# Kernel optimization log

Measured on AMD Instinct MI355X. Metric: run time of the kernel, lower is better.

The kernel has to match this reference:

```python
import jax, jax.numpy as jnp
import numpy as np

EPS = 1e-6  # eigenvalue floor before log

def _gauss_1d(sigma):
    r = int(np.ceil(3.0 * sigma))
    t = np.arange(-r, r + 1, dtype=np.float32)
    g = np.exp(-0.5 * (t / sigma) ** 2)
    g = g / g.sum()
    dg = (-t / (sigma ** 2)) * g  # derivative-of-gaussian kernel
    return jnp.asarray(g), jnp.asarray(dg)

def _conv_axis(x, k, axis):
    # x: [N, 1, D, H, W]; 1D conv along given spatial axis (2,3,4), SAME padding
    K = k.shape[0]
    wshape = [1, 1, 1, 1, 1]; wshape[axis] = K
    w = k.reshape(wshape)
    pad = [(0, 0)] * 3; pad[axis - 2] = (K // 2, K // 2)
    return jax.lax.conv_general_dilated(
        x, w, (1, 1, 1), pad,
        dimension_numbers=('NCDHW', 'OIDHW', 'NCDHW'))

def _blur3(x, g):
    return _conv_axis(_conv_axis(_conv_axis(x, g, 4), g, 3), g, 2)

def _structure_tensor(v, sigma, rho):
    # v: [B, 1, D, H, W] -> per-voxel symmetric 3x3 tensor [B, D, H, W, 3, 3]
    g_s, dg_s = _gauss_1d(sigma)
    g_r, _ = _gauss_1d(rho)
    # derivative-of-gaussian gradients (separable)
    gx = _conv_axis(_conv_axis(_conv_axis(v, dg_s, 4), g_s, 3), g_s, 2)
    gy = _conv_axis(_conv_axis(_conv_axis(v, g_s, 4), dg_s, 3), g_s, 2)
    gz = _conv_axis(_conv_axis(_conv_axis(v, g_s, 4), g_s, 3), dg_s, 2)
    # 6 unique components Sxx,Syy,Szz,Sxy,Sxz,Syz, blurred at scale rho
    comps = jnp.concatenate(
        [gx * gx, gy * gy, gz * gz, gx * gy, gx * gz, gy * gz], axis=1)  # [B,6,D,H,W]
    B, _, D, H, W = comps.shape
    comps = _blur3(comps.reshape(B * 6, 1, D, H, W), g_r).reshape(B, 6, D, H, W)
    Sxx, Syy, Szz, Sxy, Sxz, Syz = [comps[:, i] for i in range(6)]
    row0 = jnp.stack([Sxx, Sxy, Sxz], axis=-1)
    row1 = jnp.stack([Sxy, Syy, Syz], axis=-1)
    row2 = jnp.stack([Sxz, Syz, Szz], axis=-1)
    return jnp.stack([row0, row1, row2], axis=-2)  # [B,D,H,W,3,3]

def _logm_sym(M):
    # matrix log of batched symmetric 3x3 via eigendecomposition
    w, V = jnp.linalg.eigh(M)
    logw = jnp.log(jnp.maximum(w, EPS))
    return jnp.einsum('...ij,...j,...kj->...ik', V, logw, V)

def setup_inputs() -> dict:
    key = jax.random.key(0)
    k1, k2 = jax.random.split(key)
    shape = (2, 1, 96, 96, 96)
    return {
        'real_hi_res': jax.random.normal(k1, shape, dtype=jnp.float32),
        'fake_hi_res': jax.random.normal(k2, shape, dtype=jnp.float32),
    }

def reference(real_hi_res, fake_hi_res, sigma=1.0, rho=2.0):
    S_real = _structure_tensor(real_hi_res, sigma, rho)
    S_fake = _structure_tensor(fake_hi_res, sigma, rho)
    L_real = _logm_sym(S_real)
    L_fake = _logm_sym(S_fake)
    diff = L_real - L_fake
    # per-voxel squared log-Euclidean distance, mean per patch, summed over batch
    dist_points = jnp.sum(diff * diff, axis=(-2, -1))  # [B,D,H,W]
    loss = jnp.sum(jnp.mean(dist_points, axis=(1, 2, 3)))
    return loss
```

## Files before the change

### kernel.cpp

```cpp
#include <hip/hip_runtime.h>
#include <math.h>

#define DIM 96
#define HW_ 9216
#define N3 884736
#define TPB 256

template<int K> struct CW { float w[K]; };

__device__ inline float4 ld4(const float* p) { return *reinterpret_cast<const float4*>(p); }
__device__ inline void st4(float* p, float4 v) { *reinterpret_cast<float4*>(p) = v; }
__device__ inline float2 ld2(const float* p) { return *reinterpret_cast<const float2*>(p); }
__device__ inline float4 fma4(float w, float4 a, float4 acc) {
  acc.x = fmaf(w, a.x, acc.x); acc.y = fmaf(w, a.y, acc.y);
  acc.z = fmaf(w, a.z, acc.z); acc.w = fmaf(w, a.w, acc.w); return acc;
}
__device__ inline float2 fma2(float w, float2 a, float2 acc) {
  acc.x = fmaf(w, a.x, acc.x); acc.y = fmaf(w, a.y, acc.y); return acc;
}
__device__ inline int xswz(int bid, int nb) { return (bid & 7) * (nb >> 3) + (bid >> 3); }

__global__ void k1_dualW(const float* __restrict__ p0, const float* __restrict__ p1,
                         const float* __restrict__ p2, const float* __restrict__ p3,
                         float* __restrict__ A, int nvol, CW<7> g, CW<7> dg) {
  int t = blockIdx.x * TPB + threadIdx.x;
  if (t >= nvol * (N3 / 4)) return;
  int base = t * 4;
  int v = base / N3, i = base - v * N3;
  const float* src = (v == 0) ? p0 : (v == 1) ? p1 : (v == 2) ? p2 : p3;
  int x = i % DIM;
  float win[10];
#pragma unroll
  for (int u = 0; u < 10; ++u) {
    int xx = x + u - 3;
    win[u] = (0 <= xx && xx < DIM) ? src[i + u - 3] : 0.f;
  }
  float4 sa, sb;
#pragma unroll
  for (int k = 0; k < 4; ++k) {
    float a_ = 0.f, b_ = 0.f;
#pragma unroll
    for (int j = 0; j < 7; ++j) {
      float val = win[k + j];
      a_ = fmaf(g.w[j], val, a_);
      b_ = fmaf(dg.w[j], val, b_);
    }
    ((float*)&sa)[k] = a_;
    ((float*)&sb)[k] = b_;
  }
  st4(A + (size_t)(2 * v) * N3 + i, sa);
  st4(A + (size_t)(2 * v + 1) * N3 + i, sb);
}

__global__ void k2_H(const float* __restrict__ A, float* __restrict__ B,
                     int nvol, CW<7> g, CW<7> dg) {
  int t = blockIdx.x * TPB + threadIdx.x;
  if (t >= nvol * (N3 / 4)) return;
  int base = t * 4;
  int v = base / N3, i = base - v * N3;
  int h = (i / DIM) % DIM;
  const float* Wg  = A + (size_t)(2 * v) * N3;
  const float* Wdg = A + (size_t)(2 * v + 1) * N3;
  float4 t0 = {0,0,0,0}, t1 = {0,0,0,0}, t2 = {0,0,0,0};
#pragma unroll
  for (int j = -3; j <= 3; ++j) {
    int hh = h + j;
    if (0 <= hh && hh < DIM) {
      float4 a = ld4(Wg + i + j * DIM);
      t0 = fma4(g.w[j + 3], a, t0);
      t1 = fma4(dg.w[j + 3], a, t1);
      float4 b = ld4(Wdg + i + j * DIM);
      t2 = fma4(g.w[j + 3], b, t2);
    }
  }
  st4(B + (size_t)(3 * v + 0) * N3 + i, t0);
  st4(B + (size_t)(3 * v + 1) * N3 + i, t1);
  st4(B + (size_t)(3 * v + 2) * N3 + i, t2);
}

__global__ void k3_D(const float* __restrict__ B, float* __restrict__ A,
                     int nf, CW<7> g, CW<7> dg) {
  int t = xswz(blockIdx.x, gridDim.x) * TPB + threadIdx.x;
  if (t >= nf * (N3 / 4)) return;
  int base = t * 4;
  int f = base / N3;
  int d = (base / HW_) % DIM;
  bool use_dg = (f % 3 == 0);
  float4 acc = {0,0,0,0};
#pragma unroll
  for (int j = -3; j <= 3; ++j) {
    int dd = d + j;
    if (0 <= dd && dd < DIM) {
      float w = use_dg ? dg.w[j + 3] : g.w[j + 3];
      acc = fma4(w, ld4(B + base + j * HW_), acc);
    }
  }
  st4(A + base, acc);
}

__global__ void k4_prodW(const float* __restrict__ A, float* __restrict__ C,
                         int nvol, CW<13> w13) {
  int t = blockIdx.x * TPB + threadIdx.x;
  if (t >= nvol * (N3 / 4)) return;
  int base = t * 4;
  int v = base / N3, i = base - v * N3;
  const float* gz = A + (size_t)(3 * v + 0) * N3;
  const float* gy = A + (size_t)(3 * v + 1) * N3;
  const float* gx = A + (size_t)(3 * v + 2) * N3;
  int x = i % DIM;
  float wx[16], wy[16], wz[16];
#pragma unroll
  for (int u = 0; u < 16; ++u) {
    int xx = x + u - 6;
    bool ok = (0 <= xx && xx < DIM);
    wx[u] = ok ? gx[i + u - 6] : 0.f;
    wy[u] = ok ? gy[i + u - 6] : 0.f;
    wz[u] = ok ? gz[i + u - 6] : 0.f;
  }
  float4 a0 = {0,0,0,0}, a1 = {0,0,0,0}, a2 = {0,0,0,0};
  float4 a3 = {0,0,0,0}, a4 = {0,0,0,0}, a5 = {0,0,0,0};
#pragma unroll
  for (int k = 0; k < 4; ++k) {
    float s0=0,s1=0,s2=0,s3=0,s4=0,s5=0;
#pragma unroll
    for (int j = 0; j < 13; ++j) {
      float w = w13.w[j];
      float a = wx[k + j], b = wy[k + j], c = wz[k + j];
      float wa = w * a, wb = w * b, wc = w * c;
      s0 = fmaf(wa, a, s0); s3 = fmaf(wa, b, s3); s4 = fmaf(wa, c, s4);
      s1 = fmaf(wb, b, s1); s5 = fmaf(wb, c, s5);
      s2 = fmaf(wc, c, s2);
    }
    ((float*)&a0)[k]=s0; ((float*)&a1)[k]=s1; ((float*)&a2)[k]=s2;
    ((float*)&a3)[k]=s3; ((float*)&a4)[k]=s4; ((float*)&a5)[k]=s5;
  }
  float* dst = C + (size_t)(6 * v) * N3;
  st4(dst + 0*N3 + i, a0); st4(dst + 1*N3 + i, a1); st4(dst + 2*N3 + i, a2);
  st4(dst + 3*N3 + i, a3); st4(dst + 4*N3 + i, a4); st4(dst + 5*N3 + i, a5);
}

__global__ void k5_blurD(const float* __restrict__ In, float* __restrict__ Out,
                         int nf, CW<13> w13) {
  int t = xswz(blockIdx.x, gridDim.x) * TPB + threadIdx.x;
  if (t >= nf * (N3 / 4)) return;
  int base = t * 4;
  int d = (base / HW_) % DIM;
  float4 acc = {0,0,0,0};
#pragma unroll
  for (int j = -6; j <= 6; ++j) {
    int dd = d + j;
    if (0 <= dd && dd < DIM)
      acc = fma4(w13.w[j + 6], ld4(In + base + j * HW_), acc);
  }
  st4(Out + base, acc);
}

template<int P, int Q, int RR>
__device__ inline void jrot(float a[3][3], float V[3][3]) {
  float apq = a[P][Q];
  if (apq != 0.f) {
    float app = a[P][P], aqq = a[Q][Q];
    float theta = 0.5f * (aqq - app) / apq;
    float t = 1.f / (fabsf(theta) + sqrtf(theta * theta + 1.f));
    t = (theta >= 0.f) ? t : -t;
    float c = rsqrtf(t * t + 1.f);
    float s = t * c;
    a[P][P] = app - t * apq;
    a[Q][Q] = aqq + t * apq;
    a[P][Q] = 0.f; a[Q][P] = 0.f;
    float arp = a[RR][P], arq = a[RR][Q];
    float nrp = c * arp - s * arq;
    float nrq = s * arp + c * arq;
    a[RR][P] = nrp; a[P][RR] = nrp;
    a[RR][Q] = nrq; a[Q][RR] = nrq;
#pragma unroll
    for (int r = 0; r < 3; ++r) {
      float vp = V[r][P], vq = V[r][Q];
      V[r][P] = c * vp - s * vq;
      V[r][Q] = s * vp + c * vq;
    }
  }
}

__device__ inline void logm3(const float s6[6], float L[6]) {
  float a[3][3] = {{s6[0], s6[3], s6[4]},
                   {s6[3], s6[1], s6[5]},
                   {s6[4], s6[5], s6[2]}};
  float V[3][3] = {{1,0,0},{0,1,0},{0,0,1}};
#pragma unroll
  for (int sw = 0; sw < 4; ++sw) {
    jrot<0,1,2>(a, V);
    jrot<0,2,1>(a, V);
    jrot<1,2,0>(a, V);
  }
  float l0 = logf(fmaxf(a[0][0], 1e-6f));
  float l1 = logf(fmaxf(a[1][1], 1e-6f));
  float l2 = logf(fmaxf(a[2][2], 1e-6f));
  L[0] = l0*V[0][0]*V[0][0] + l1*V[0][1]*V[0][1] + l2*V[0][2]*V[0][2];
  L[1] = l0*V[1][0]*V[1][0] + l1*V[1][1]*V[1][1] + l2*V[1][2]*V[1][2];
  L[2] = l0*V[2][0]*V[2][0] + l1*V[2][1]*V[2][1] + l2*V[2][2]*V[2][2];
  L[3] = l0*V[0][0]*V[1][0] + l1*V[0][1]*V[1][1] + l2*V[0][2]*V[1][2];
  L[4] = l0*V[0][0]*V[2][0] + l1*V[0][1]*V[2][1] + l2*V[0][2]*V[2][2];
  L[5] = l0*V[1][0]*V[2][0] + l1*V[1][1]*V[2][1] + l2*V[1][2]*V[2][2];
}

__global__ void k6_fused(const float* __restrict__ Sr, const float* __restrict__ Sf,
                         size_t strideElems, int nb, float* __restrict__ out,
                         CW<13> w13) {
  int t = xswz(blockIdx.x, gridDim.x) * TPB + threadIdx.x;
  float val = 0.f;
  if (t < nb * (N3 / 2)) {
    int b = t / (N3 / 2);
    int base = (t - b * (N3 / 2)) * 2;
    int h = (base / DIM) % DIM;
    const float* sR = Sr + (size_t)b * strideElems;
    const float* sF = Sf + (size_t)b * strideElems;
    float2 sr[6], sf[6];
#pragma unroll
    for (int c = 0; c < 6; ++c) {
      float2 ar = {0,0}, af = {0,0};
#pragma unroll
      for (int j = -6; j <= 6; ++j) {
        int hh = h + j;
        if (0 <= hh && hh < DIM) {
          float w = w13.w[j + 6];
          ar = fma2(w, ld2(sR + (size_t)c * N3 + base + j * DIM), ar);
          af = fma2(w, ld2(sF + (size_t)c * N3 + base + j * DIM), af);
        }
      }
      sr[c] = ar; sf[c] = af;
    }
#pragma unroll
    for (int k = 0; k < 2; ++k) {
      float s6r[6], s6f[6], Lr[6], Lf[6];
#pragma unroll
      for (int c = 0; c < 6; ++c) {
        s6r[c] = ((const float*)&sr[c])[k];
        s6f[c] = ((const float*)&sf[c])[k];
      }
      logm3(s6r, Lr);
      logm3(s6f, Lf);
      float d0 = Lr[0]-Lf[0], d1 = Lr[1]-Lf[1], d2 = Lr[2]-Lf[2];
      float d3 = Lr[3]-Lf[3], d4 = Lr[4]-Lf[4], d5 = Lr[5]-Lf[5];
      val += d0*d0 + d1*d1 + d2*d2 + 2.f*(d3*d3 + d4*d4 + d5*d5);
    }
  }
#pragma unroll
  for (int off = 32; off > 0; off >>= 1) val += __shfl_down(val, off, 64);
  __shared__ float sm[TPB / 64];
  int wave = threadIdx.x >> 6;
  if ((threadIdx.x & 63) == 0) sm[wave] = val;
  __syncthreads();
  if (threadIdx.x == 0) {
    float s = 0.f;
#pragma unroll
    for (int wv = 0; wv < TPB / 64; ++wv) s += sm[wv];
    atomicAdd(out, s * (1.0f / (float)N3));
  }
}

extern "C" void kernel_launch(void* const* d_in, const int* in_sizes, int n_in,
                              void* d_out, int out_size, void* d_ws, size_t ws_size,
                              hipStream_t stream) {
  const float* real = (const float*)d_in[0];
  const float* fake = (const float*)d_in[1];
  float* out = (float*)d_out;

  CW<7> g7, d7;
  CW<13> g13;
  {
    double g[7], sum = 0.0;
    for (int i = 0; i < 7; ++i) { double t = i - 3; g[i] = exp(-0.5 * t * t); sum += g[i]; }
    for (int i = 0; i < 7; ++i) {
      double gn = g[i] / sum;
      g7.w[i] = (float)gn;
      d7.w[i] = (float)(-(double)(i - 3) * gn);
    }
    double h[13], s2 = 0.0;
    for (int i = 0; i < 13; ++i) { double t = (i - 6) / 2.0; h[i] = exp(-0.5 * t * t); s2 += h[i]; }
    for (int i = 0; i < 13; ++i) g13.w[i] = (float)(h[i] / s2);
  }

  hipMemsetAsync(d_out, 0, sizeof(float) * (size_t)out_size, stream);

  const size_t FLD = (size_t)N3;
  float* W = (float*)d_ws;

  const size_t need_fused = 48 * FLD * sizeof(float);
  if (ws_size >= need_fused) {
    float* A = W;
    float* B = A + 12 * FLD;
    float* C = B + 12 * FLD;
    const int gV  = 4 * (N3 / 4) / TPB;
    const int g12 = 12 * (N3 / 4) / TPB;
    const int g24 = 24 * (N3 / 4) / TPB;
    const int g6  = 2 * (N3 / 2) / TPB;

    k1_dualW<<<gV,  TPB, 0, stream>>>(real, fake, real + N3, fake + N3, A, 4, g7, d7);
    k2_H    <<<gV,  TPB, 0, stream>>>(A, B, 4, g7, d7);
    k3_D    <<<g12, TPB, 0, stream>>>(B, A, 12, g7, d7);
    k4_prodW<<<gV,  TPB, 0, stream>>>(A, C, 4, g13);
    k5_blurD<<<g24, TPB, 0, stream>>>(C, W, 24, g13);
    k6_fused<<<g6,  TPB, 0, stream>>>(W, W + 6 * FLD, 12 * FLD, 2, out, g13);
  } else {
    float* P0 = W;
    float* P1 = P0 + 6 * FLD;
    float* P2 = P1 + 6 * FLD;
    const int gV  = 2 * (N3 / 4) / TPB;
    const int g6  = 6 * (N3 / 4) / TPB;
    const int gK6 = 1 * (N3 / 2) / TPB;

    for (int b = 0; b < 2; ++b) {
      const float* rv = real + (size_t)b * N3;
      const float* fv = fake + (size_t)b * N3;
      k1_dualW<<<gV, TPB, 0, stream>>>(rv, fv, rv, fv, P0, 2, g7, d7);
      k2_H    <<<gV, TPB, 0, stream>>>(P0, P1, 2, g7, d7);
      k3_D    <<<g6, TPB, 0, stream>>>(P1, P0, 6, g7, d7);
      k4_prodW<<<gV, TPB, 0, stream>>>(P0, P1, 2, g13);
      k5_blurD<<<g6, TPB, 0, stream>>>(P1, P0, 6, g13);
      k5_blurD<<<g6, TPB, 0, stream>>>(P2, P1, 6, g13);
      k6_fused<<<gK6, TPB, 0, stream>>>(P0, P1, 0, 1, out, g13);
    }
  }
}
```

Baseline: 382.1 us.

## Replace Jacobi eigensolver with closed-form eigenvalues and Sylvester polynomial logm

Replaces the 4-sweep Jacobi rotation eigendecomposition in the per-voxel 3x3 matrix log with closed-form trigonometric eigenvalues. The log is then built as a quadratic matrix polynomial in S using divided differences, so no eigenvectors are needed. This removes many divisions, square roots and data-dependent branches from the fused logm kernel. It relies on fast intrinsics (__cosf, __logf, __frcp_rn) and fallback branches for near-degenerate eigenvalues, which adds some risk to numerical accuracy.

Result: faster. 354.1 us (-7.3%).

```diff
diff --git a/kernel.cpp b/kernel.cpp
--- a/kernel.cpp
+++ b/kernel.cpp
@@ -5,6 +5,7 @@
 #define HW_ 9216
 #define N3 884736
 #define TPB 256
+#define EPSF 1e-6f
 
 template<int K> struct CW { float w[K]; };
 
@@ -155,53 +156,61 @@
   st4(Out + base, acc);
 }
 
-template<int P, int Q, int RR>
-__device__ inline void jrot(float a[3][3], float V[3][3]) {
-  float apq = a[P][Q];
-  if (apq != 0.f) {
-    float app = a[P][P], aqq = a[Q][Q];
-    float theta = 0.5f * (aqq - app) / apq;
-    float t = 1.f / (fabsf(theta) + sqrtf(theta * theta + 1.f));
-    t = (theta >= 0.f) ? t : -t;
-    float c = rsqrtf(t * t + 1.f);
-    float s = t * c;
-    a[P][P] = app - t * apq;
-    a[Q][Q] = aqq + t * apq;
-    a[P][Q] = 0.f; a[Q][P] = 0.f;
-    float arp = a[RR][P], arq = a[RR][Q];
-    float nrp = c * arp - s * arq;
-    float nrq = s * arp + c * arq;
-    a[RR][P] = nrp; a[P][RR] = nrp;
-    a[RR][Q] = nrq; a[Q][RR] = nrq;
-#pragma unroll
-    for (int r = 0; r < 3; ++r) {
-      float vp = V[r][P], vq = V[r][Q];
-      V[r][P] = c * vp - s * vq;
-      V[r][Q] = s * vp + c * vq;
-    }
-  }
-}
-
 __device__ inline void logm3(const float s6[6], float L[6]) {
-  float a[3][3] = {{s6[0], s6[3], s6[4]},
-                   {s6[3], s6[1], s6[5]},
-                   {s6[4], s6[5], s6[2]}};
-  float V[3][3] = {{1,0,0},{0,1,0},{0,0,1}};
-#pragma unroll
-  for (int sw = 0; sw < 4; ++sw) {
-    jrot<0,1,2>(a, V);
-    jrot<0,2,1>(a, V);
-    jrot<1,2,0>(a, V);
-  }
-  float l0 = logf(fmaxf(a[0][0], 1e-6f));
-  float l1 = logf(fmaxf(a[1][1], 1e-6f));
-  float l2 = logf(fmaxf(a[2][2], 1e-6f));
-  L[0] = l0*V[0][0]*V[0][0] + l1*V[0][1]*V[0][1] + l2*V[0][2]*V[0][2];
-  L[1] = l0*V[1][0]*V[1][0] + l1*V[1][1]*V[1][1] + l2*V[1][2]*V[1][2];
-  L[2] = l0*V[2][0]*V[2][0] + l1*V[2][1]*V[2][1] + l2*V[2][2]*V[2][2];
-  L[3] = l0*V[0][0]*V[1][0] + l1*V[0][1]*V[1][1] + l2*V[0][2]*V[1][2];
-  L[4] = l0*V[0][0]*V[2][0] + l1*V[0][1]*V[2][1] + l2*V[0][2]*V[2][2];
-  L[5] = l0*V[1][0]*V[2][0] + l1*V[1][1]*V[2][1] + l2*V[1][2]*V[2][2];
+  const float Sxx=s6[0], Syy=s6[1], Szz=s6[2], Sxy=s6[3], Sxz=s6[4], Syz=s6[5];
+  float q  = (Sxx + Syy + Szz) * (1.f/3.f);
+  float p1 = Sxy*Sxy + Sxz*Sxz + Syz*Syz;
+  float axx = Sxx - q, ayy = Syy - q, azz = Szz - q;
+  float p2 = axx*axx + ayy*ayy + azz*azz + 2.f*p1;
+  float l0, l1, l2;
+  if (p2 < 1e-24f) {
+    l0 = l1 = l2 = q;
+  } else {
+    float p  = sqrtf(p2 * (1.f/6.f));
+    float ip = __frcp_rn(p);
+    float bxx=axx*ip, byy=ayy*ip, bzz=azz*ip;
+    float bxy=Sxy*ip, bxz=Sxz*ip, byz=Syz*ip;
+    float detB = bxx*(byy*bzz - byz*byz) - bxy*(bxy*bzz - byz*bxz)
+               + bxz*(bxy*byz - byy*bxz);
+    float r = fminf(1.f, fmaxf(-1.f, 0.5f * detB));
+    float phi = acosf(r) * (1.f/3.f);
+    float c_a = __cosf(phi);
+    float c_c = __cosf(phi + 2.0943951023931953f);
+    l0 = q + 2.f*p*c_a;
+    l2 = q + 2.f*p*c_c;
+    l1 = 3.f*q - l0 - l2;
+  }
+  float f0 = __logf(fmaxf(l0, EPSF));
+  float f1 = __logf(fmaxf(l1, EPSF));
+  float f2 = __logf(fmaxf(l2, EPSF));
+  float d01 = l0 - l1, d12 = l1 - l2, d02 = l0 - l2;
+  float mag = fmaxf(fabsf(l0), fabsf(l2));
+  float thr = 1e-6f + 1e-4f * mag;
+  float g01 = (d01 > thr) ? (f0 - f1) * __frcp_rn(d01)
+                          : ((l0 > EPSF) ? 2.f * __frcp_rn(l0 + l1) : 0.f);
+  float g12 = (d12 > thr) ? (f1 - f2) * __frcp_rn(d12)
+                          : ((l1 > EPSF) ? 2.f * __frcp_rn(l1 + l2) : 0.f);
+  float c2;
+  if (d02 > thr) {
+    c2 = (g01 - g12) * __frcp_rn(d02);
+  } else {
+    float m = fmaxf((l0 + l1 + l2) * (1.f/3.f), EPSF);
+    c2 = (l2 > EPSF) ? -0.5f * __frcp_rn(m * m) : 0.f;
+  }
+  float c1 = g01 - c2 * (l0 + l1);
+  float c0 = f0 - g01 * l0 + c2 * l0 * l1;
+  float m2xx = Sxx*Sxx + Sxy*Sxy + Sxz*Sxz;
+  float m2yy = Sxy*Sxy + Syy*Syy + Syz*Syz;
+  float m2zz = Sxz*Sxz + Syz*Syz + Szz*Szz;
+  float m2xy = Sxy*(Sxx + Syy) + Sxz*Syz;
+  float m2xz = Sxz*(Sxx + Szz) + Sxy*Syz;
+  float m2yz = Syz*(Syy + Szz) + Sxy*Sxz;
+  L[0] = c0 + c1*Sxx + c2*m2xx;
+  L[1] = c0 + c1*Syy + c2*m2yy;
+  L[2] = c0 + c1*Szz + c2*m2zz;
+  L[3] = c1*Sxy + c2*m2xy;
+  L[4] = c1*Sxz + c2*m2xz;
+  L[5] = c1*Syz + c2*m2yz;
 }
 
 __global__ void k6_fused(const float* __restrict__ Sr, const float* __restrict__ Sf,
```
